# Kernel tuning notes

Measured on AMD Instinct MI355X. Metric: run time of the kernel, lower is better.

## Reference

```python
import jax, jax.numpy as jnp
import numpy as np

B, T_IN, T_OUT, D, U, L = 32, 256, 256, 128, 256, 3
STDDEV, MEAN = 0.01, 0.0
SQRT3 = 1.732051


def _cell(x, h, W, Urec, b):
    # Keras GRUCell, reset_after=True (default). b: [2, 3U] (input bias, recurrent bias)
    gx = x @ W + b[0]
    gh = h @ Urec + b[1]
    xz, xr, xn = jnp.split(gx, 3, axis=-1)
    hz, hr, hn = jnp.split(gh, 3, axis=-1)
    z = jax.nn.sigmoid(xz + hz)
    r = jax.nn.sigmoid(xr + hr)
    n = jnp.tanh(xn + r * hn)
    return z * h + (1.0 - z) * n


def setup_inputs() -> dict:
    key = jax.random.key(0)
    ks = jax.random.split(key, 16)
    inputs = jax.random.normal(ks[0], (B, T_IN, D), dtype=jnp.float32)
    # uniform noise in [mean - sqrt(3)*std, mean + sqrt(3)*std], matching self.noise_kwargs
    noise = jax.random.uniform(ks[1], (B, T_IN, D), dtype=jnp.float32,
                               minval=MEAN - SQRT3 * STDDEV, maxval=MEAN + SQRT3 * STDDEV)
    s = 0.05
    h_init = jax.random.normal(ks[2], (L, U), dtype=jnp.float32)  # learnable_state vars, N(0,1)
    W0 = jax.random.normal(ks[3], (D, 3 * U), dtype=jnp.float32) * s
    U0 = jax.random.normal(ks[4], (U, 3 * U), dtype=jnp.float32) * s
    b0 = jax.random.normal(ks[5], (2, 3 * U), dtype=jnp.float32) * s
    W1 = jax.random.normal(ks[6], (U, 3 * U), dtype=jnp.float32) * s
    U1 = jax.random.normal(ks[7], (U, 3 * U), dtype=jnp.float32) * s
    b1 = jax.random.normal(ks[8], (2, 3 * U), dtype=jnp.float32) * s
    W2 = jax.random.normal(ks[9], (U, 3 * U), dtype=jnp.float32) * s
    U2 = jax.random.normal(ks[10], (U, 3 * U), dtype=jnp.float32) * s
    b2 = jax.random.normal(ks[11], (2, 3 * U), dtype=jnp.float32) * s
    Wd = jax.random.normal(ks[12], (U, D), dtype=jnp.float32) * s
    bd = jnp.zeros((D,), dtype=jnp.float32)
    return {"inputs": inputs, "noise": noise, "h_init": h_init,
            "W0": W0, "U0": U0, "b0": b0, "W1": W1, "U1": U1, "b1": b1,
            "W2": W2, "U2": U2, "b2": b2, "Wd": Wd, "bd": bd}


def reference(inputs, noise, h_init, W0, U0, b0, W1, U1, b1, W2, U2, b2, Wd, bd):
    params = ((W0, U0, b0), (W1, U1, b1), (W2, U2, b2))
    batch = inputs.shape[0]
    units = U0.shape[0]

    def stack_step(states, x):
        new = []
        h = _cell(x, states[0], *params[0]); new.append(h); x = h  # no residual on layer 0
        for j in range(1, L):
            h = _cell(x, states[j], *params[j]); new.append(h); x = h + x  # residual
        return tuple(new), x

    # initial states: tiled learnable vectors
    states0 = tuple(jnp.tile(h_init[j][None, :], (batch, 1)) for j in range(L))
    xs = jnp.transpose(inputs + noise, (1, 0, 2))  # [T_in, B, D], noise only in warmup

    def warm(carry, x):
        states, _ = carry
        states, xtop = stack_step(states, x)
        return (states, xtop), None

    (states, xtop), _ = jax.lax.scan(warm, (states0, jnp.zeros((batch, units), inputs.dtype)), xs)
    pred0 = xtop @ Wd + bd  # dense, linear activation

    def ar(carry, _):
        states, pred = carry
        states, xtop = stack_step(states, pred)
        pred = xtop @ Wd + bd
        return (states, pred), pred

    (_, _), preds = jax.lax.scan(ar, (states, pred0), None, length=T_OUT - 1)
    preds = jnp.concatenate([pred0[None], preds], axis=0)  # [T_out, B, D]
    return jnp.transpose(preds, (1, 0, 2))  # [B, T_out, D]
```

## Files before the change

kernel.cpp:

```cpp
#include <hip/hip_runtime.h>
#include <math.h>

#define T_IN   256
#define T_OUT  256
#define D_     128
#define U_     256
#define NSTEP  511

#define NWG    16
#define NCH    2
#define NGRP   16
#define THREADS 256

#define G64_H0   0
#define G64_H1   512
#define G64_H2   1024
#define G64_PD   1536
#define GRPSTRIDE64 10240
#define WS_NEED  (NGRP * GRPSTRIDE64 * 8)

typedef _Float16 half8 __attribute__((ext_vector_type(8)));
typedef float    f32x4 __attribute__((ext_vector_type(4)));

__device__ __forceinline__ float sigmoidf_(float x) { return 1.0f / (1.0f + __expf(-x)); }
__device__ __forceinline__ unsigned pk(float a, float b) {
    union { _Float16 h[2]; unsigned u; } v;
    v.h[0] = (_Float16)a; v.h[1] = (_Float16)b; return v.u;
}
__device__ __forceinline__ float2 upk(unsigned x) {
    union { unsigned u; _Float16 h[2]; } v; v.u = x;
    return make_float2((float)v.h[0], (float)v.h[1]);
}

__global__ void zero_ws(unsigned* p, int n) {
    int i = blockIdx.x * 256 + threadIdx.x;
    if (i < n) p[i] = 0;
}

__device__ __forceinline__ f32x4 mm_k(const unsigned* xb, const _Float16* wb,
                                      int nks, f32x4 acc) {
    #pragma unroll
    for (int ks = 0; ks < nks; ++ks) {
        half8 a = *(const half8*)(const void*)(xb + ks * 16);
        half8 b = *(const half8*)(const void*)(wb + ks * 32);
        acc = __builtin_amdgcn_mfma_f32_16x16x32_f16(a, b, acc, 0, 0, 0);
    }
    return acc;
}

__global__ __launch_bounds__(THREADS) void gru_dist(
    const float* __restrict__ inputs, const float* __restrict__ noise,
    const float* __restrict__ h_init,
    const float* __restrict__ W0, const float* __restrict__ U0, const float* __restrict__ b0,
    const float* __restrict__ W1, const float* __restrict__ U1, const float* __restrict__ b1,
    const float* __restrict__ W2, const float* __restrict__ U2, const float* __restrict__ b2,
    const float* __restrict__ Wd, const float* __restrict__ bd,
    unsigned long long* __restrict__ ws, float* __restrict__ out)
{
    const int bid  = blockIdx.x;
    const int grp  = bid & 15;
    const int w    = bid >> 4;
    const int t    = threadIdx.x;
    const int lane = t & 63;
    const int wv   = t >> 6;
    const int u16  = lane & 15, kg = lane >> 4, ch2 = u16 & 1;

    __shared__ __align__(16) _Float16 lw0[48 * 136];
    __shared__ __align__(16) _Float16 lu0[48 * 264];
    __shared__ __align__(16) _Float16 lw1[48 * 264];
    __shared__ __align__(16) _Float16 lu1[48 * 264];
    __shared__ __align__(16) _Float16 lw2[48 * 264];
    __shared__ __align__(16) _Float16 lu2[48 * 264];
    __shared__ __align__(16) _Float16 lwdk[128 * 32];
    __shared__ __align__(16) _Float16 sxd[16 * 32];
    __shared__ __align__(16) unsigned sx0[NCH][68];
    __shared__ __align__(16) unsigned sh0[2][NCH][132];
    __shared__ __align__(16) unsigned sh1[NCH][132];
    __shared__ __align__(16) unsigned sh2[NCH][132];
    __shared__ __align__(16) unsigned sx2[NCH][132];
    __shared__ float sgx[3][192];
    __shared__ float sgh[3][192];
    __shared__ float sb[3][2][48];
    __shared__ float sbdf[128];
    __shared__ float spredf[NCH][128];

    unsigned long long* gbase = ws + (size_t)grp * GRPSTRIDE64;
    unsigned long long* g_h0 = gbase + G64_H0;
    unsigned long long* g_h1 = gbase + G64_H1;
    unsigned long long* g_h2 = gbase + G64_H2;
    unsigned long long* g_pd = gbase + G64_PD;

    {
        const float* srcs[6] = {W0, U0, W1, U1, W2, U2};
        _Float16*    dsts[6] = {lw0, lu0, lw1, lu1, lw2, lu2};
        const int Ks[6] = {128, 256, 256, 256, 256, 256};
        const int Ss[6] = {136, 264, 264, 264, 264, 264};
        for (int m = 0; m < 6; ++m) {
            const float* s = srcs[m]; _Float16* d = dsts[m];
            const int K = Ks[m], S = Ss[m];
            for (int idx = t; idx < 48 * K; idx += THREADS) {
                int c = idx / K, k = idx - c * K;
                int g = ((c >> 4) << 8) + (w << 4) + (c & 15);
                d[c * S + k] = (_Float16)s[k * 768 + g];
            }
        }
        for (int idx = t; idx < 128 * 32; idx += THREADS) {
            int n = idx >> 5, k = idx & 31;
            lwdk[idx] = (k < 16) ? (_Float16)Wd[(w * 16 + k) * 128 + n] : (_Float16)0.f;
        }
        for (int idx = t; idx < 16 * 32; idx += THREADS) sxd[idx] = (_Float16)0.f;
        const float* bsrc[3] = {b0, b1, b2};
        for (int idx = t; idx < 288; idx += THREADS) {
            int l = idx / 96, r = idx - l * 96, which = r / 48, c = r - which * 48;
            int g = ((c >> 4) << 8) + (w << 4) + (c & 15);
            sb[l][which][c] = bsrc[l][which * 768 + g];
        }
        for (int idx = t; idx < 128; idx += THREADS) sbdf[idx] = bd[idx];
        for (int idx = t; idx < 2 * 128; idx += THREADS) {
            int cc = idx >> 7, p = idx & 127;
            unsigned v0 = pk(h_init[0 * 256 + 2 * p], h_init[0 * 256 + 2 * p + 1]);
            sh0[0][cc][p] = v0; sh0[1][cc][p] = v0;
            sh1[cc][p] = pk(h_init[1 * 256 + 2 * p], h_init[1 * 256 + 2 * p + 1]);
            sh2[cc][p] = pk(h_init[2 * 256 + 2 * p], h_init[2 * 256 + 2 * p + 1]);
        }
    }
    float hrA = 0.f, hrB = 0.f;
    if (t < 48) {
        int l = t >> 4, pl = t & 7;
        hrA = h_init[l * 256 + (w * 16 + 2 * pl)];
        hrB = h_init[l * 256 + (w * 16 + 2 * pl) + 1];
    }
    __syncthreads();

    auto gather_tagged = [&](const unsigned long long* garr, unsigned (*lds)[132],
                             unsigned tag) {
        const unsigned long long* base = garr + (tag & 1) * 256;
        for (int idx = t; idx < 240; idx += THREADS) {
            int i = idx >> 4, rem = idx & 15, cc = rem >> 3, pl = rem & 7;
            int src = i + (i >= w);
            int gpi = src * 8 + pl;
            const unsigned long long* p = base + cc * 128 + gpi;
            unsigned long long v = __hip_atomic_load(p, __ATOMIC_RELAXED,
                                                     __HIP_MEMORY_SCOPE_AGENT);
            unsigned it = 0;
            while ((unsigned)(v >> 32) < tag) {
                __builtin_amdgcn_s_sleep(1);
                v = __hip_atomic_load(p, __ATOMIC_RELAXED, __HIP_MEMORY_SCOPE_AGENT);
                if (++it > (1u << 20)) break;
            }
            lds[cc][gpi] = (unsigned)v;
        }
    };
    auto store_g = [&](int l, f32x4 wa, f32x4 ua) {
        if (lane < 16) {
            #pragma unroll
            for (int r = 0; r < 2; ++r) {
                sgx[l][(wv * 16 + u16) * 4 + r] = wa[r];
                sgh[l][(wv * 16 + u16) * 4 + r] = ua[r];
            }
        }
    };
    auto do_final = [&](int l, unsigned (*ldst)[132], unsigned long long* garr,
                        unsigned tag, bool dox3) {
        if ((t >> 4) == l) {
            int cc = (t >> 3) & 1, pl = t & 7, gpi = w * 8 + pl;
            float hn2[2];
            float hcur[2] = {hrA, hrB};
            #pragma unroll
            for (int i = 0; i < 2; ++i) {
                int lu = 2 * pl + i;
                float gxz = sgx[l][(0 * 16 + lu) * 4 + cc] + sb[l][0][lu];
                float ghz = sgh[l][(0 * 16 + lu) * 4 + cc] + sb[l][1][lu];
                float gxr = sgx[l][(1 * 16 + lu) * 4 + cc] + sb[l][0][16 + lu];
                float ghr = sgh[l][(1 * 16 + lu) * 4 + cc] + sb[l][1][16 + lu];
                float gxn = sgx[l][(2 * 16 + lu) * 4 + cc] + sb[l][0][32 + lu];
                float ghn = sgh[l][(2 * 16 + lu) * 4 + cc] + sb[l][1][32 + lu];
                float z = sigmoidf_(gxz + ghz);
                float r = sigmoidf_(gxr + ghr);
                float n = tanhf(gxn + r * ghn);
                hn2[i] = z * hcur[i] + (1.f - z) * n;
            }
            hrA = hn2[0]; hrB = hn2[1];
            unsigned pv = pk(hn2[0], hn2[1]);
            ldst[cc][gpi] = pv;
            __hip_atomic_store(garr + (tag & 1) * 256 + cc * 128 + gpi,
                               ((unsigned long long)tag << 32) | (unsigned long long)pv,
                               __ATOMIC_RELAXED, __HIP_MEMORY_SCOPE_AGENT);
            if (dox3) {
                float2 x2p = upk(sx2[cc][gpi]);
                sxd[cc * 32 + 2 * pl]     = (_Float16)(hn2[0] + x2p.x);
                sxd[cc * 32 + 2 * pl + 1] = (_Float16)(hn2[1] + x2p.y);
            }
        }
    };
    auto dense_pub = [&](unsigned tag) {
        half8 a = *(const half8*)(const void*)(sxd + u16 * 32 + kg * 8);
        int nt0 = 2 * wv;
        half8 bA = *(const half8*)(const void*)(lwdk + (nt0 * 16 + u16) * 32 + kg * 8);
        half8 bB = *(const half8*)(const void*)(lwdk + ((nt0 + 1) * 16 + u16) * 32 + kg * 8);
        f32x4 z4l = {0.f, 0.f, 0.f, 0.f};
        f32x4 dA = __builtin_amdgcn_mfma_f32_16x16x32_f16(a, bA, z4l, 0, 0, 0);
        f32x4 dB = __builtin_amdgcn_mfma_f32_16x16x32_f16(a, bB, z4l, 0, 0, 0);
        if (lane < 16) {
            unsigned long long* base = g_pd + (tag & 1) * 4096 + (unsigned)w * 256;
            #pragma unroll
            for (int r = 0; r < 2; ++r) {
                union { float f; unsigned u; } cA, cB;
                cA.f = dA[r]; cB.f = dB[r];
                __hip_atomic_store(base + r * 128 + nt0 * 16 + u16,
                                   ((unsigned long long)tag << 32) | cA.u,
                                   __ATOMIC_RELAXED, __HIP_MEMORY_SCOPE_AGENT);
                __hip_atomic_store(base + r * 128 + (nt0 + 1) * 16 + u16,
                                   ((unsigned long long)tag << 32) | cB.u,
                                   __ATOMIC_RELAXED, __HIP_MEMORY_SCOPE_AGENT);
            }
        }
    };
    auto pred_gather = [&](unsigned tag, int row) {
        const int cc = t >> 7, o = t & 127;
        const unsigned long long* base = g_pd + (tag & 1) * 4096 + cc * 128 + o;
        unsigned long long v[16];
        #pragma unroll
        for (int src = 0; src < 16; ++src)
            v[src] = __hip_atomic_load(base + src * 256, __ATOMIC_RELAXED,
                                       __HIP_MEMORY_SCOPE_AGENT);
        #pragma unroll
        for (int src = 0; src < 16; ++src) {
            unsigned it = 0;
            while ((unsigned)(v[src] >> 32) < tag) {
                __builtin_amdgcn_s_sleep(1);
                v[src] = __hip_atomic_load(base + src * 256, __ATOMIC_RELAXED,
                                           __HIP_MEMORY_SCOPE_AGENT);
                if (++it > (1u << 20)) break;
            }
        }
        float s = sbdf[o];
        #pragma unroll
        for (int src = 0; src < 16; ++src) {
            union { unsigned u; float f; } cv; cv.u = (unsigned)v[src];
            s += cv.f;
        }
        spredf[cc][o] = s;
        __syncthreads();
        if (t < 128) {
            int c2 = t >> 6, p2 = t & 63;
            sx0[c2][p2] = pk(spredf[c2][2 * p2], spredf[c2][2 * p2 + 1]);
        }
        if (t < 16) {
            int c2 = t >> 3, dd = w * 8 + (t & 7);
            out[((size_t)(grp * NCH + c2) * T_OUT + row) * D_ + dd] = spredf[c2][dd];
        }
    };

    const f32x4 z4 = {0.f, 0.f, 0.f, 0.f};
    f32x4 ua0 = z4, ua1 = z4, ua2 = z4;

    if (t < 128) {
        int cc = t >> 6, p = t & 63;
        const float* ip = inputs + ((size_t)(grp * NCH + cc) * T_IN + 0) * D_ + 2 * p;
        const float* np = noise  + ((size_t)(grp * NCH + cc) * T_IN + 0) * D_ + 2 * p;
        sx0[cc][p] = pk(ip[0] + np[0], ip[1] + np[1]);
    }
    __syncthreads();

    for (int b = 0; b <= 257; ++b) {
        const int pcur = b & 1, pprev = (b + 1) & 1;
        if (wv < 3) {
            if (b < 256) {
                f32x4 wa = mm_k(&sx0[0][0] + ch2 * 68 + kg * 4,
                                lw0 + (wv * 16 + u16) * 136 + kg * 8, 4, z4);
                f32x4 ua = mm_k(&sh0[pprev][0][0] + ch2 * 132 + kg * 4,
                                lu0 + (wv * 16 + u16) * 264 + kg * 8, 8, z4);
                store_g(0, wa, ua);
            }
            if (b >= 1 && b <= 256) {
                f32x4 wa = mm_k(&sh0[pprev][0][0] + ch2 * 132 + kg * 4,
                                lw1 + (wv * 16 + u16) * 264 + kg * 8, 8, z4);
                f32x4 ua = mm_k(&sh1[0][0] + ch2 * 132 + kg * 4,
                                lu1 + (wv * 16 + u16) * 264 + kg * 8, 8, z4);
                store_g(1, wa, ua);
            }
            if (b >= 2) {
                f32x4 wa = mm_k(&sx2[0][0] + ch2 * 132 + kg * 4,
                                lw2 + (wv * 16 + u16) * 264 + kg * 8, 8, z4);
                f32x4 ua = mm_k(&sh2[0][0] + ch2 * 132 + kg * 4,
                                lu2 + (wv * 16 + u16) * 264 + kg * 8, 8, z4);
                store_g(2, wa, ua);
            }
        }
        __syncthreads();
        if (b < 256)            do_final(0, sh0[pcur], g_h0, (unsigned)(b + 1), false);
        if (b >= 1 && b <= 256) do_final(1, sh1, g_h1, (unsigned)b, false);
        if (b >= 2)             do_final(2, sh2, g_h2, (unsigned)(b - 1), b == 257);
        float i0 = 0.f, i1 = 0.f;
        if (b + 1 < 256 && t < 128) {
            int cc = t >> 6, p = t & 63;
            const float* ip = inputs + ((size_t)(grp * NCH + cc) * T_IN + (b + 1)) * D_ + 2 * p;
            const float* np = noise  + ((size_t)(grp * NCH + cc) * T_IN + (b + 1)) * D_ + 2 * p;
            i0 = ip[0] + np[0]; i1 = ip[1] + np[1];
        }
        if (b < 256)            gather_tagged(g_h0, sh0[pcur], (unsigned)(b + 1));
        if (b >= 1 && b <= 256) gather_tagged(g_h1, sh1, (unsigned)b);
        if (b >= 2)             gather_tagged(g_h2, sh2, (unsigned)(b - 1));
        if (b + 1 < 256 && t < 128) sx0[t >> 6][t & 63] = pk(i0, i1);
        __syncthreads();
        if (b >= 1 && b <= 256) {
            int cc = t >> 7, p = t & 127;
            float2 a = upk(sh0[pprev][cc][p]);
            float2 bb = upk(sh1[cc][p]);
            sx2[cc][p] = pk(a.x + bb.x, a.y + bb.y);
            __syncthreads();
        }
        if (b == 257) {
            dense_pub(1);
            if (wv < 3)
                ua0 = mm_k(&sh0[1][0][0] + ch2 * 132 + kg * 4,
                           lu0 + (wv * 16 + u16) * 264 + kg * 8, 8, z4);
            pred_gather(1, 0);
            __syncthreads();
        }
    }

    for (int ts = T_IN; ts < NSTEP; ++ts) {
        const unsigned ht = (unsigned)(ts + 1);
        const unsigned pt = (unsigned)(ts - 254);
        if (wv < 3) {
            f32x4 wa = mm_k(&sx0[0][0] + ch2 * 68 + kg * 4,
                            lw0 + (wv * 16 + u16) * 136 + kg * 8, 4, z4);
            store_g(0, wa, ua0);
        }
        __syncthreads();
        do_final(0, sh0[1], g_h0, ht, false);
        if (wv < 3)
            ua1 = mm_k(&sh1[0][0] + ch2 * 132 + kg * 4,
                       lu1 + (wv * 16 + u16) * 264 + kg * 8, 8, z4);
        gather_tagged(g_h2, sh2, ht - 1);
        gather_tagged(g_h0, sh0[1], ht);
        __syncthreads();
        if (wv < 3) {
            f32x4 wa = mm_k(&sh0[1][0][0] + ch2 * 132 + kg * 4,
                            lw1 + (wv * 16 + u16) * 264 + kg * 8, 8, z4);
            store_g(1, wa, ua1);
        }
        __syncthreads();
        do_final(1, sh1, g_h1, ht, false);
        if (wv < 3)
            ua2 = mm_k(&sh2[0][0] + ch2 * 132 + kg * 4,
                       lu2 + (wv * 16 + u16) * 264 + kg * 8, 8, z4);
        gather_tagged(g_h1, sh1, ht);
        __syncthreads();
        {
            int cc = t >> 7, p = t & 127;
            float2 a = upk(sh0[1][cc][p]);
            float2 bb = upk(sh1[cc][p]);
            sx2[cc][p] = pk(a.x + bb.x, a.y + bb.y);
        }
        __syncthreads();
        if (wv < 3) {
            f32x4 wa = mm_k(&sx2[0][0] + ch2 * 132 + kg * 4,
                            lw2 + (wv * 16 + u16) * 264 + kg * 8, 8, z4);
            store_g(2, wa, ua2);
        }
        __syncthreads();
        do_final(2, sh2, g_h2, ht, true);
        __syncthreads();
        dense_pub(pt);
        if (wv < 3)
            ua0 = mm_k(&sh0[1][0][0] + ch2 * 132 + kg * 4,
                       lu0 + (wv * 16 + u16) * 264 + kg * 8, 8, z4);
        pred_gather(pt, ts - 255);
        __syncthreads();
    }
}

__global__ __launch_bounds__(768) void gru_ar_fp32(
    const float* __restrict__ inputs, const float* __restrict__ noise,
    const float* __restrict__ h_init,
    const float* __restrict__ W0, const float* __restrict__ U0, const float* __restrict__ b0,
    const float* __restrict__ W1, const float* __restrict__ U1, const float* __restrict__ b1,
    const float* __restrict__ W2, const float* __restrict__ U2, const float* __restrict__ b2,
    const float* __restrict__ Wd, const float* __restrict__ bd,
    float* __restrict__ out)
{
    const int b = blockIdx.x;
    const int j = threadIdx.x;
    __shared__ float s_x[U_];
    __shared__ float s_h[3][U_];
    __shared__ float s_gz[U_], s_gr[U_], s_gxn[U_], s_ghn[U_];
    __shared__ float s_pred[D_];
    if (j < U_) {
        s_h[0][j] = h_init[0 * U_ + j];
        s_h[1][j] = h_init[1 * U_ + j];
        s_h[2][j] = h_init[2 * U_ + j];
    }
    __syncthreads();
    const float* Ws[3]  = {W0, W1, W2};
    const float* Us[3]  = {U0, U1, U2};
    const float* bss[3] = {b0, b1, b2};
    for (int ts = 0; ts < NSTEP; ++ts) {
        if (j < D_) {
            if (ts < T_IN) {
                const int idx = (b * T_IN + ts) * D_ + j;
                s_x[j] = inputs[idx] + noise[idx];
            } else s_x[j] = s_pred[j];
        }
        __syncthreads();
        #pragma unroll
        for (int l = 0; l < 3; ++l) {
            const int K = (l == 0) ? D_ : U_;
            const float* W = Ws[l]; const float* Urec = Us[l]; const float* bias = bss[l];
            float gx = bias[j];
            for (int k = 0; k < K; ++k) gx = fmaf(s_x[k], W[k * 768 + j], gx);
            float gh = bias[768 + j];
            for (int k = 0; k < U_; ++k) gh = fmaf(s_h[l][k], Urec[k * 768 + j], gh);
            if (j < U_)            s_gz[j] = gx + gh;
            else if (j < 2 * U_)   s_gr[j - U_] = gx + gh;
            else { s_gxn[j - 2 * U_] = gx; s_ghn[j - 2 * U_] = gh; }
            __syncthreads();
            if (j < U_) {
                const float z = sigmoidf_(s_gz[j]);
                const float r = sigmoidf_(s_gr[j]);
                const float n = tanhf(s_gxn[j] + r * s_ghn[j]);
                const float h_new = z * s_h[l][j] + (1.0f - z) * n;
                s_h[l][j] = h_new;
                s_x[j] = (l == 0) ? h_new : (h_new + s_x[j]);
            }
            __syncthreads();
        }
        if (ts >= T_IN - 1) {
            if (j < D_) {
                float p = bd[j];
                for (int k = 0; k < U_; ++k) p = fmaf(s_x[k], Wd[k * D_ + j], p);
                s_pred[j] = p;
                out[(b * T_OUT + (ts - (T_IN - 1))) * D_ + j] = p;
            }
            __syncthreads();
        }
    }
}

extern "C" void kernel_launch(void* const* d_in, const int* in_sizes, int n_in,
                              void* d_out, int out_size, void* d_ws, size_t ws_size,
                              hipStream_t stream) {
    (void)in_sizes; (void)n_in; (void)out_size;
    const float* inputs = (const float*)d_in[0];
    const float* noise  = (const float*)d_in[1];
    const float* h_init = (const float*)d_in[2];
    const float* W0 = (const float*)d_in[3];
    const float* U0 = (const float*)d_in[4];
    const float* b0 = (const float*)d_in[5];
    const float* W1 = (const float*)d_in[6];
    const float* U1 = (const float*)d_in[7];
    const float* b1 = (const float*)d_in[8];
    const float* W2 = (const float*)d_in[9];
    const float* U2 = (const float*)d_in[10];
    const float* b2 = (const float*)d_in[11];
    const float* Wd = (const float*)d_in[12];
    const float* bd = (const float*)d_in[13];
    float* out = (float*)d_out;

    if (ws_size >= (size_t)WS_NEED) {
        const int n = NGRP * GRPSTRIDE64 * 2;
        zero_ws<<<(n + 255) / 256, 256, 0, stream>>>((unsigned*)d_ws, n);
        gru_dist<<<NGRP * NWG, THREADS, 0, stream>>>(
            inputs, noise, h_init, W0, U0, b0, W1, U1, b1, W2, U2, b2, Wd, bd,
            (unsigned long long*)d_ws, out);
    } else {
        gru_ar_fp32<<<32, 768, 0, stream>>>(
            inputs, noise, h_init, W0, U0, b0, W1, U1, b1, W2, U2, b2, Wd, bd, out);
    }
}
```

Measured before the change: 3.058 ms.

## Issue cross-workgroup state loads before local matmuls to overlap polling latency

Replaces the serial tagged-gather helper with inline code. All atomic loads for the needed hidden-state slices are issued first, the independent recurrent matmul runs next, and only then does the code spin on the tags. The prediction gather gets the same treatment, and the residual sum for layer 2 input is fused into the layer-1 gather and the final step, removing one barrier per step. This targets the global-memory round-trip latency on the cross-workgroup exchange, at the cost of more registers and duplicated code.

```diff
diff --git a/kernel.cpp b/kernel.cpp
--- a/kernel.cpp
+++ b/kernel.cpp
@@ -132,25 +132,6 @@
     }
     __syncthreads();
 
-    auto gather_tagged = [&](const unsigned long long* garr, unsigned (*lds)[132],
-                             unsigned tag) {
-        const unsigned long long* base = garr + (tag & 1) * 256;
-        for (int idx = t; idx < 240; idx += THREADS) {
-            int i = idx >> 4, rem = idx & 15, cc = rem >> 3, pl = rem & 7;
-            int src = i + (i >= w);
-            int gpi = src * 8 + pl;
-            const unsigned long long* p = base + cc * 128 + gpi;
-            unsigned long long v = __hip_atomic_load(p, __ATOMIC_RELAXED,
-                                                     __HIP_MEMORY_SCOPE_AGENT);
-            unsigned it = 0;
-            while ((unsigned)(v >> 32) < tag) {
-                __builtin_amdgcn_s_sleep(1);
-                v = __hip_atomic_load(p, __ATOMIC_RELAXED, __HIP_MEMORY_SCOPE_AGENT);
-                if (++it > (1u << 20)) break;
-            }
-            lds[cc][gpi] = (unsigned)v;
-        }
-    };
     auto store_g = [&](int l, f32x4 wa, f32x4 ua) {
         if (lane < 16) {
             #pragma unroll
@@ -161,7 +142,7 @@
         }
     };
     auto do_final = [&](int l, unsigned (*ldst)[132], unsigned long long* garr,
-                        unsigned tag, bool dox3) {
+                        unsigned tag, bool dox3, bool dox2) {
         if ((t >> 4) == l) {
             int cc = (t >> 3) & 1, pl = t & 7, gpi = w * 8 + pl;
             float hn2[2];
@@ -186,6 +167,10 @@
             __hip_atomic_store(garr + (tag & 1) * 256 + cc * 128 + gpi,
                                ((unsigned long long)tag << 32) | (unsigned long long)pv,
                                __ATOMIC_RELAXED, __HIP_MEMORY_SCOPE_AGENT);
+            if (dox2) {
+                float2 h0p = upk(sh0[1][cc][gpi]);
+                sx2[cc][gpi] = pk(hn2[0] + h0p.x, hn2[1] + h0p.y);
+            }
             if (dox3) {
                 float2 x2p = upk(sx2[cc][gpi]);
                 sxd[cc * 32 + 2 * pl]     = (_Float16)(hn2[0] + x2p.x);
@@ -289,9 +274,9 @@
             }
         }
         __syncthreads();
-        if (b < 256)            do_final(0, sh0[pcur], g_h0, (unsigned)(b + 1), false);
-        if (b >= 1 && b <= 256) do_final(1, sh1, g_h1, (unsigned)b, false);
-        if (b >= 2)             do_final(2, sh2, g_h2, (unsigned)(b - 1), b == 257);
+        if (b < 256)            do_final(0, sh0[pcur], g_h0, (unsigned)(b + 1), false, false);
+        if (b >= 1 && b <= 256) do_final(1, sh1, g_h1, (unsigned)b, false, false);
+        if (b >= 2)             do_final(2, sh2, g_h2, (unsigned)(b - 1), b == 257, false);
         float i0 = 0.f, i1 = 0.f;
         if (b + 1 < 256 && t < 128) {
             int cc = t >> 6, p = t & 63;
@@ -299,9 +284,54 @@
             const float* np = noise  + ((size_t)(grp * NCH + cc) * T_IN + (b + 1)) * D_ + 2 * p;
             i0 = ip[0] + np[0]; i1 = ip[1] + np[1];
         }
-        if (b < 256)            gather_tagged(g_h0, sh0[pcur], (unsigned)(b + 1));
-        if (b >= 1 && b <= 256) gather_tagged(g_h1, sh1, (unsigned)b);
-        if (b >= 2)             gather_tagged(g_h2, sh2, (unsigned)(b - 1));
+        {
+            const bool act = (t < 240);
+            const bool n0 = act && (b < 256);
+            const bool n1 = act && (b >= 1 && b <= 256);
+            const bool n2 = act && (b >= 2);
+            int cc = 0, gpi = 0;
+            const unsigned long long *p0 = nullptr, *p1 = nullptr, *p2 = nullptr;
+            unsigned long long v0 = 0, v1 = 0, v2 = 0;
+            if (act) {
+                int i = t >> 4, rem = t & 15; cc = rem >> 3; int pl = rem & 7;
+                int src = i + (i >= w);
+                gpi = src * 8 + pl;
+                const int off = cc * 128 + gpi;
+                if (n0) { p0 = g_h0 + (((unsigned)(b + 1)) & 1) * 256 + off;
+                          v0 = __hip_atomic_load(p0, __ATOMIC_RELAXED, __HIP_MEMORY_SCOPE_AGENT); }
+                if (n1) { p1 = g_h1 + (((unsigned)b) & 1) * 256 + off;
+                          v1 = __hip_atomic_load(p1, __ATOMIC_RELAXED, __HIP_MEMORY_SCOPE_AGENT); }
+                if (n2) { p2 = g_h2 + (((unsigned)(b - 1)) & 1) * 256 + off;
+                          v2 = __hip_atomic_load(p2, __ATOMIC_RELAXED, __HIP_MEMORY_SCOPE_AGENT); }
+            }
+            if (n0) {
+                unsigned it = 0;
+                while ((unsigned)(v0 >> 32) < (unsigned)(b + 1)) {
+                    __builtin_amdgcn_s_sleep(1);
+                    v0 = __hip_atomic_load(p0, __ATOMIC_RELAXED, __HIP_MEMORY_SCOPE_AGENT);
+                    if (++it > (1u << 20)) break;
+                }
+                sh0[pcur][cc][gpi] = (unsigned)v0;
+            }
+            if (n1) {
+                unsigned it = 0;
+                while ((unsigned)(v1 >> 32) < (unsigned)b) {
+                    __builtin_amdgcn_s_sleep(1);
+                    v1 = __hip_atomic_load(p1, __ATOMIC_RELAXED, __HIP_MEMORY_SCOPE_AGENT);
+                    if (++it > (1u << 20)) break;
+                }
+                sh1[cc][gpi] = (unsigned)v1;
+            }
+            if (n2) {
+                unsigned it = 0;
+                while ((unsigned)(v2 >> 32) < (unsigned)(b - 1)) {
+                    __builtin_amdgcn_s_sleep(1);
+                    v2 = __hip_atomic_load(p2, __ATOMIC_RELAXED, __HIP_MEMORY_SCOPE_AGENT);
+                    if (++it > (1u << 20)) break;
+                }
+                sh2[cc][gpi] = (unsigned)v2;
+            }
+        }
         if (b + 1 < 256 && t < 128) sx0[t >> 6][t & 63] = pk(i0, i1);
         __syncthreads();
         if (b >= 1 && b <= 256) {
@@ -330,12 +360,42 @@
             store_g(0, wa, ua0);
         }
         __syncthreads();
-        do_final(0, sh0[1], g_h0, ht, false);
-        if (wv < 3)
-            ua1 = mm_k(&sh1[0][0] + ch2 * 132 + kg * 4,
-                       lu1 + (wv * 16 + u16) * 264 + kg * 8, 8, z4);
-        gather_tagged(g_h2, sh2, ht - 1);
-        gather_tagged(g_h0, sh0[1], ht);
+        do_final(0, sh0[1], g_h0, ht, false, false);
+        {
+            const bool act = (t < 240);
+            int cc = 0, gpi = 0;
+            const unsigned long long *pA = nullptr, *pB = nullptr;
+            unsigned long long vA = 0, vB = 0;
+            if (act) {
+                int i = t >> 4, rem = t & 15; cc = rem >> 3; int pl = rem & 7;
+                int src = i + (i >= w);
+                gpi = src * 8 + pl;
+                const int off = cc * 128 + gpi;
+                pA = g_h2 + ((ht - 1) & 1) * 256 + off;
+                pB = g_h0 + (ht & 1) * 256 + off;
+                vA = __hip_atomic_load(pA, __ATOMIC_RELAXED, __HIP_MEMORY_SCOPE_AGENT);
+                vB = __hip_atomic_load(pB, __ATOMIC_RELAXED, __HIP_MEMORY_SCOPE_AGENT);
+            }
+            if (wv < 3)
+                ua1 = mm_k(&sh1[0][0] + ch2 * 132 + kg * 4,
+                           lu1 + (wv * 16 + u16) * 264 + kg * 8, 8, z4);
+            if (act) {
+                unsigned it = 0;
+                while ((unsigned)(vA >> 32) < ht - 1) {
+                    __builtin_amdgcn_s_sleep(1);
+                    vA = __hip_atomic_load(pA, __ATOMIC_RELAXED, __HIP_MEMORY_SCOPE_AGENT);
+                    if (++it > (1u << 20)) break;
+                }
+                sh2[cc][gpi] = (unsigned)vA;
+                it = 0;
+                while ((unsigned)(vB >> 32) < ht) {
+                    __builtin_amdgcn_s_sleep(1);
+                    vB = __hip_atomic_load(pB, __ATOMIC_RELAXED, __HIP_MEMORY_SCOPE_AGENT);
+                    if (++it > (1u << 20)) break;
+                }
+                sh0[1][cc][gpi] = (unsigned)vB;
+            }
+        }
         __syncthreads();
         if (wv < 3) {
             f32x4 wa = mm_k(&sh0[1][0][0] + ch2 * 132 + kg * 4,
@@ -343,17 +403,34 @@
             store_g(1, wa, ua1);
         }
         __syncthreads();
-        do_final(1, sh1, g_h1, ht, false);
-        if (wv < 3)
-            ua2 = mm_k(&sh2[0][0] + ch2 * 132 + kg * 4,
-                       lu2 + (wv * 16 + u16) * 264 + kg * 8, 8, z4);
-        gather_tagged(g_h1, sh1, ht);
-        __syncthreads();
+        do_final(1, sh1, g_h1, ht, false, true);
         {
-            int cc = t >> 7, p = t & 127;
-            float2 a = upk(sh0[1][cc][p]);
-            float2 bb = upk(sh1[cc][p]);
-            sx2[cc][p] = pk(a.x + bb.x, a.y + bb.y);
+            const bool act = (t < 240);
+            int cc = 0, gpi = 0;
+            const unsigned long long* pB = nullptr;
+            unsigned long long vB = 0;
+            if (act) {
+                int i = t >> 4, rem = t & 15; cc = rem >> 3; int pl = rem & 7;
+                int src = i + (i >= w);
+                gpi = src * 8 + pl;
+                pB = g_h1 + (ht & 1) * 256 + cc * 128 + gpi;
+                vB = __hip_atomic_load(pB, __ATOMIC_RELAXED, __HIP_MEMORY_SCOPE_AGENT);
+            }
+            if (wv < 3)
+                ua2 = mm_k(&sh2[0][0] + ch2 * 132 + kg * 4,
+                           lu2 + (wv * 16 + u16) * 264 + kg * 8, 8, z4);
+            if (act) {
+                unsigned it = 0;
+                while ((unsigned)(vB >> 32) < ht) {
+                    __builtin_amdgcn_s_sleep(1);
+                    vB = __hip_atomic_load(pB, __ATOMIC_RELAXED, __HIP_MEMORY_SCOPE_AGENT);
+                    if (++it > (1u << 20)) break;
+                }
+                sh1[cc][gpi] = (unsigned)vB;
+                float2 a = upk((unsigned)vB);
+                float2 b0 = upk(sh0[1][cc][gpi]);
+                sx2[cc][gpi] = pk(a.x + b0.x, a.y + b0.y);
+            }
         }
         __syncthreads();
         if (wv < 3) {
@@ -362,13 +439,47 @@
             store_g(2, wa, ua2);
         }
         __syncthreads();
-        do_final(2, sh2, g_h2, ht, true);
+        do_final(2, sh2, g_h2, ht, true, false);
         __syncthreads();
         dense_pub(pt);
-        if (wv < 3)
-            ua0 = mm_k(&sh0[1][0][0] + ch2 * 132 + kg * 4,
-                       lu0 + (wv * 16 + u16) * 264 + kg * 8, 8, z4);
-        pred_gather(pt, ts - 255);
+        {
+            const int cc = t >> 7, o = t & 127;
+            const unsigned long long* base = g_pd + (pt & 1) * 4096 + cc * 128 + o;
+            unsigned long long v[16];
+            #pragma unroll
+            for (int src = 0; src < 16; ++src)
+                v[src] = __hip_atomic_load(base + src * 256, __ATOMIC_RELAXED,
+                                           __HIP_MEMORY_SCOPE_AGENT);
+            if (wv < 3)
+                ua0 = mm_k(&sh0[1][0][0] + ch2 * 132 + kg * 4,
+                           lu0 + (wv * 16 + u16) * 264 + kg * 8, 8, z4);
+            #pragma unroll
+            for (int src = 0; src < 16; ++src) {
+                unsigned it = 0;
+                while ((unsigned)(v[src] >> 32) < pt) {
+                    __builtin_amdgcn_s_sleep(1);
+                    v[src] = __hip_atomic_load(base + src * 256, __ATOMIC_RELAXED,
+                                               __HIP_MEMORY_SCOPE_AGENT);
+                    if (++it > (1u << 20)) break;
+                }
+            }
+            float s = sbdf[o];
+            #pragma unroll
+            for (int src = 0; src < 16; ++src) {
+                union { unsigned u; float f; } cv; cv.u = (unsigned)v[src];
+                s += cv.f;
+            }
+            spredf[cc][o] = s;
+            __syncthreads();
+            if (t < 128) {
+                int c2 = t >> 6, p2 = t & 63;
+                sx0[c2][p2] = pk(spredf[c2][2 * p2], spredf[c2][2 * p2 + 1]);
+            }
+            if (t < 16) {
+                int c2 = t >> 3, dd = w * 8 + (t & 7);
+                out[((size_t)(grp * NCH + c2) * T_OUT + (ts - 255)) * D_ + dd] = spredf[c2][dd];
+            }
+        }
         __syncthreads();
     }
 }
```

Result: slower. 3.540 ms (+15.7%).
